# Kernel tuning notes

Measured on AMD Instinct MI355X. Metric: run time of the kernel, lower is better.

The kernel has to match this reference:

```python
import jax, jax.numpy as jnp
import numpy as np

B, N, K, D, H = 4, 8192, 16, 128, 4
DK = D // H  # key_dim = num_hiddens // num_heads
NEG_INF = -1e9


def setup_inputs() -> dict:
    key = jax.random.key(0)
    ks = jax.random.split(key, 16)
    s = 1.0 / np.sqrt(D)
    return {
        "vertex_feat": jax.random.normal(ks[0], (B, N, D), dtype=jnp.float32),
        "neighbors_idx": jax.random.randint(ks[1], (B, N, K), 0, N, dtype=jnp.int32),
        "valid_lens": jax.random.randint(ks[2], (B, N), 0, K, dtype=jnp.int32),
        # MultiHeadAttention projections (keras EinsumDense with bias)
        "Wq": (jax.random.normal(ks[3], (D, H, DK)) * s).astype(jnp.float32),
        "bq": jnp.zeros((H, DK), jnp.float32),
        "Wk": (jax.random.normal(ks[4], (D, H, DK)) * s).astype(jnp.float32),
        "bk": jnp.zeros((H, DK), jnp.float32),
        "Wv": (jax.random.normal(ks[5], (D, H, DK)) * s).astype(jnp.float32),
        "bv": jnp.zeros((H, DK), jnp.float32),
        "Wo": (jax.random.normal(ks[6], (H, DK, D)) * s).astype(jnp.float32),
        "bo": jnp.zeros((D,), jnp.float32),
        # MLP: Dense(D, relu) -> Dense(D)
        "W1": (jax.random.normal(ks[7], (D, D)) * s).astype(jnp.float32),
        "b1": jnp.zeros((D,), jnp.float32),
        "W2": (jax.random.normal(ks[8], (D, D)) * s).astype(jnp.float32),
        "b2": jnp.zeros((D,), jnp.float32),
    }


def reference(vertex_feat, neighbors_idx, valid_lens,
              Wq, bq, Wk, bk, Wv, bv, Wo, bo, W1, b1, W2, b2):
    # query: [B, N, 1, D]; gathered neighbors (batch_dims=1): [B, N, K, D]
    q = vertex_feat[:, :, None, :]
    neigh = jax.vmap(lambda vf, idx: vf[idx])(vertex_feat, neighbors_idx)
    value = jnp.concatenate([q, neigh], axis=2)  # [B, N, K+1, D]

    # per-head projections
    qh = jnp.einsum('bnqd,dhk->bnqhk', q, Wq) + bq      # [B,N,1,H,DK]
    kh = jnp.einsum('bnsd,dhk->bnshk', value, Wk) + bk  # [B,N,K+1,H,DK]
    vh = jnp.einsum('bnsd,dhk->bnshk', value, Wv) + bv

    # attention over the neighbor axis (attention_axes=(2,))
    scores = jnp.einsum('bnqhk,bnshk->bnhqs', qh, kh) / np.sqrt(DK)  # [B,N,H,1,K+1]
    # mask: positions < valid_lens + 1 (self + valid neighbors)
    pos = jnp.arange(K + 1)[None, None, :]                # [1,1,K+1]
    mask = pos < (valid_lens + 1)[:, :, None]             # [B,N,K+1] bool
    scores = scores + jnp.where(mask, 0.0, NEG_INF)[:, :, None, None, :]
    attn = jax.nn.softmax(scores, axis=-1)                # [B,N,H,1,K+1]

    ctx = jnp.einsum('bnhqs,bnshk->bnqhk', attn, vh)      # [B,N,1,H,DK]
    out = jnp.einsum('bnqhk,hkd->bnqd', ctx, Wo) + bo     # [B,N,1,D]
    out = out[:, :, 0, :]                                  # squeeze -> [B,N,D]

    # MLP (dropout inactive at inference)
    h = jax.nn.relu(out @ W1 + b1)
    new_vertex_feat = h @ W2 + b2
    return new_vertex_feat
```

## Files before the change

kernel.cpp:

```cpp
#include <hip/hip_runtime.h>
#include <math.h>

#define BB 4
#define NN 8192
#define KNB 16
#define DD 128
#define SS 17
#define M_TOT (BB*NN)
#define WPAD 136

typedef __attribute__((ext_vector_type(8))) short          bf8;
typedef __attribute__((ext_vector_type(4))) float          f4;
typedef __attribute__((ext_vector_type(4))) unsigned short u16x4;

static __device__ __forceinline__ unsigned short f2bf(float f) {
    unsigned u = __builtin_bit_cast(unsigned, f);
    u += 0x7fffu + ((u >> 16) & 1u);
    return (unsigned short)(u >> 16);
}
static __device__ __forceinline__ float bf2f(unsigned short h) {
    return __builtin_bit_cast(float, (unsigned)h << 16);
}
static __device__ __forceinline__ float bf2f_s(short h) {
    return __builtin_bit_cast(float, (unsigned)(unsigned short)h << 16);
}

__global__ __launch_bounds__(256) void cvt_wT(
    const float* __restrict__ Wq, const float* __restrict__ Wk,
    const float* __restrict__ Wv, const float* __restrict__ Wo,
    const float* __restrict__ W1, const float* __restrict__ W2,
    unsigned short* __restrict__ out)
{
    int m = blockIdx.x >> 4;
    const float* src = (m == 0) ? Wq : (m == 1) ? Wk : (m == 2) ? Wv
                     : (m == 3) ? Wo : (m == 4) ? W1 : W2;
    unsigned short* dst = out + m * 16384;
    int o = (blockIdx.x & 15) * 1024 + threadIdx.x * 4;
    int n = o >> 7, k = o & 127;
    u16x4 r;
    #pragma unroll
    for (int i = 0; i < 4; ++i) r[i] = f2bf(src[(size_t)(k + i) * 128 + n]);
    *(u16x4*)(dst + o) = r;
}

__global__ __launch_bounds__(256) void qkv_kernel(
    const float* __restrict__ X, const unsigned short* __restrict__ WtT,
    const float* __restrict__ bq, const float* __restrict__ bk,
    const float* __restrict__ bv,
    unsigned short* __restrict__ qh, unsigned short* __restrict__ kh,
    unsigned short* __restrict__ vh)
{
    __shared__ unsigned short Xs[64 * WPAD];
    __shared__ unsigned short Wb[128 * WPAD];

    const int tid  = threadIdx.x;
    const int row0 = blockIdx.x * 64;

    {
        const float4* Xg = (const float4*)(X + (size_t)row0 * DD);
        #pragma unroll
        for (int i = 0; i < 8; ++i) {
            int idx = tid + i * 256;
            int r = idx >> 5, c4 = idx & 31;
            float4 v = Xg[idx];
            u16x4 u;
            u[0] = f2bf(v.x); u[1] = f2bf(v.y); u[2] = f2bf(v.z); u[3] = f2bf(v.w);
            *(u16x4*)(Xs + r * WPAD + c4 * 4) = u;
        }
    }
    #pragma unroll
    for (int i = 0; i < 8; ++i) {
        int c = tid + i * 256;
        int n = c >> 4, k8 = c & 15;
        *(bf8*)(Wb + n * WPAD + k8 * 8) = ((const bf8*)WtT)[c];
    }

    const int lane = tid & 63, wv = tid >> 6;
    const int ln = lane & 15, quad = lane >> 4;
    __syncthreads();

    bf8 afr[4];
    #pragma unroll
    for (int s = 0; s < 4; ++s)
        afr[s] = *(const bf8*)(Xs + (wv * 16 + ln) * WPAD + s * 32 + quad * 8);

    const float* biases[3] = { bq, bk, bv };
    unsigned short* outs[3] = { qh, kh, vh };

    #pragma unroll 1
    for (int g = 0; g < 3; ++g) {
        if (g > 0) {
            __syncthreads();
            const bf8* Wn = (const bf8*)(WtT + g * 16384);
            #pragma unroll
            for (int i = 0; i < 8; ++i) {
                int c = tid + i * 256;
                int n = c >> 4, k8 = c & 15;
                *(bf8*)(Wb + n * WPAD + k8 * 8) = Wn[c];
            }
            __syncthreads();
        }

        f4 acc[8] = {};
        #pragma unroll
        for (int t = 0; t < 8; ++t) {
            bf8 bfr[4];
            #pragma unroll
            for (int s = 0; s < 4; ++s)
                bfr[s] = *(const bf8*)(Wb + (t * 16 + ln) * WPAD + s * 32 + quad * 8);
            #pragma unroll
            for (int s = 0; s < 4; ++s)
                acc[t] = __builtin_amdgcn_mfma_f32_16x16x32_bf16(afr[s], bfr[s], acc[t], 0, 0, 0);
        }

        const float* bias = biases[g];
        unsigned short* Y = outs[g];
        #pragma unroll
        for (int t = 0; t < 8; ++t) {
            int col = t * 16 + ln;
            float bc = bias[col];
            #pragma unroll
            for (int r = 0; r < 4; ++r) {
                int row = row0 + wv * 16 + quad * 4 + r;
                Y[(size_t)row * DD + col] = f2bf(acc[t][r] + bc);
            }
        }
    }
}

__global__ __launch_bounds__(256) void attn_kernel(
    const unsigned short* __restrict__ Qh, const unsigned short* __restrict__ Kh,
    const unsigned short* __restrict__ Vh, const int* __restrict__ nbr,
    const int* __restrict__ vlen, unsigned short* __restrict__ Ctx)
{
    const int tid  = threadIdx.x;
    const int vloc = tid >> 4;
    const int ln   = tid & 15;
    const int blk  = blockIdx.x;
    const int b    = (blk & 7) >> 1;
    const int j    = ((blk >> 3) << 1) | (blk & 1);
    const int v    = b * NN + j * 16 + vloc;

    bf8 q8 = *(const bf8*)(Qh + (size_t)v * DD + ln * 8);
    float qf[8];
    #pragma unroll
    for (int i = 0; i < 8; ++i) qf[i] = bf2f_s(q8[i]);

    int rows[SS];
    rows[0] = v;
    {
        const int4* np = (const int4*)(nbr + (size_t)v * KNB);
        #pragma unroll
        for (int i = 0; i < 4; ++i) {
            int4 n4 = np[i];
            rows[1 + i * 4 + 0] = b * NN + n4.x;
            rows[1 + i * 4 + 1] = b * NN + n4.y;
            rows[1 + i * 4 + 2] = b * NN + n4.z;
            rows[1 + i * 4 + 3] = b * NN + n4.w;
        }
    }

    float sc[SS];
    #pragma unroll
    for (int s = 0; s < SS; ++s) {
        bf8 k8 = *(const bf8*)(Kh + (size_t)rows[s] * DD + ln * 8);
        float p = 0.f;
        #pragma unroll
        for (int i = 0; i < 8; ++i) p = fmaf(qf[i], bf2f_s(k8[i]), p);
        p += __shfl_xor(p, 1, 4);
        p += __shfl_xor(p, 2, 4);
        sc[s] = p * 0.17677669529663687f;
    }

    const int len = vlen[v];
    float m = sc[0];
    #pragma unroll
    for (int s = 1; s < SS; ++s) m = (s <= len) ? fmaxf(m, sc[s]) : m;
    float sum = 0.f;
    #pragma unroll
    for (int s = 0; s < SS; ++s) {
        float e = (s <= len) ? __expf(sc[s] - m) : 0.f;
        sc[s] = e;
        sum += e;
    }
    const float inv = 1.f / sum;

    float acc[8] = {};
    #pragma unroll
    for (int s = 0; s < SS; ++s) {
        bf8 v8 = *(const bf8*)(Vh + (size_t)rows[s] * DD + ln * 8);
        float w = sc[s] * inv;
        #pragma unroll
        for (int i = 0; i < 8; ++i) acc[i] = fmaf(w, bf2f_s(v8[i]), acc[i]);
    }
    bf8 r;
    #pragma unroll
    for (int i = 0; i < 8; ++i) r[i] = (short)f2bf(acc[i]);
    *(bf8*)(Ctx + (size_t)v * DD + ln * 8) = r;
}

__global__ __launch_bounds__(256) void ffn_kernel(
    const unsigned short* __restrict__ Ctxg, const unsigned short* __restrict__ WtT3,
    const float* __restrict__ bo, const float* __restrict__ b1,
    const float* __restrict__ b2, float* __restrict__ Out)
{
    __shared__ unsigned short Ct[64 * WPAD];
    __shared__ unsigned short Wb[128 * WPAD];

    const int tid  = threadIdx.x;
    const int row0 = blockIdx.x * 64;

    {
        const bf8* Cg = (const bf8*)(Ctxg + (size_t)row0 * DD);
        #pragma unroll
        for (int i = 0; i < 4; ++i) {
            int idx = tid + i * 256;
            int r = idx >> 4, c8 = idx & 15;
            *(bf8*)(Ct + r * WPAD + c8 * 8) = Cg[idx];
        }
    }
    #pragma unroll
    for (int i = 0; i < 8; ++i) {
        int c = tid + i * 256;
        int n = c >> 4, k8 = c & 15;
        *(bf8*)(Wb + n * WPAD + k8 * 8) = ((const bf8*)WtT3)[c];
    }

    const int lane = tid & 63, wv = tid >> 6;
    const int ln = lane & 15, quad = lane >> 4;
    const float* biases[3] = { bo, b1, b2 };
    __syncthreads();

    #pragma unroll 1
    for (int g = 0; g < 3; ++g) {
        bf8 afr[4];
        #pragma unroll
        for (int s = 0; s < 4; ++s)
            afr[s] = *(const bf8*)(Ct + (wv * 16 + ln) * WPAD + s * 32 + quad * 8);

        f4 acc[8] = {};
        #pragma unroll
        for (int t = 0; t < 8; ++t) {
            bf8 bfr[4];
            #pragma unroll
            for (int s = 0; s < 4; ++s)
                bfr[s] = *(const bf8*)(Wb + (t * 16 + ln) * WPAD + s * 32 + quad * 8);
            #pragma unroll
            for (int s = 0; s < 4; ++s)
                acc[t] = __builtin_amdgcn_mfma_f32_16x16x32_bf16(afr[s], bfr[s], acc[t], 0, 0, 0);
        }

        __syncthreads();

        const float* bias = biases[g];
        if (g == 2) {
            #pragma unroll
            for (int t = 0; t < 8; ++t) {
                int col = t * 16 + ln;
                float bc = bias[col];
                #pragma unroll
                for (int r = 0; r < 4; ++r) {
                    int row = row0 + wv * 16 + quad * 4 + r;
                    Out[(size_t)row * DD + col] = acc[t][r] + bc;
                }
            }
        } else {
            const bf8* Wn = (const bf8*)(WtT3 + (g + 1) * 16384);
            #pragma unroll
            for (int i = 0; i < 8; ++i) {
                int c = tid + i * 256;
                int n = c >> 4, k8 = c & 15;
                *(bf8*)(Wb + n * WPAD + k8 * 8) = Wn[c];
            }
            #pragma unroll
            for (int t = 0; t < 8; ++t) {
                int col = t * 16 + ln;
                float bc = bias[col];
                #pragma unroll
                for (int r = 0; r < 4; ++r) {
                    int rloc = wv * 16 + quad * 4 + r;
                    float vv = acc[t][r] + bc;
                    if (g == 1) vv = fmaxf(vv, 0.f);
                    Ct[rloc * WPAD + col] = f2bf(vv);
                }
            }
            __syncthreads();
        }
    }
}

extern "C" void kernel_launch(void* const* d_in, const int* in_sizes, int n_in,
                              void* d_out, int out_size, void* d_ws, size_t ws_size,
                              hipStream_t stream)
{
    const float* vf   = (const float*)d_in[0];
    const int*   nbr  = (const int*)  d_in[1];
    const int*   vlen = (const int*)  d_in[2];
    const float* Wq   = (const float*)d_in[3];
    const float* bq   = (const float*)d_in[4];
    const float* Wk   = (const float*)d_in[5];
    const float* bk   = (const float*)d_in[6];
    const float* Wv   = (const float*)d_in[7];
    const float* bv   = (const float*)d_in[8];
    const float* Wo   = (const float*)d_in[9];
    const float* bo   = (const float*)d_in[10];
    const float* W1   = (const float*)d_in[11];
    const float* b1   = (const float*)d_in[12];
    const float* W2   = (const float*)d_in[13];
    const float* b2   = (const float*)d_in[14];

    float* out = (float*)d_out;

    const size_t SZ = (size_t)M_TOT * DD;
    unsigned short* WtT = (unsigned short*)d_ws;
    unsigned short* qh  = WtT + 6 * 16384;
    unsigned short* kh  = qh + SZ;
    unsigned short* vh  = kh + SZ;
    unsigned short* ctx = vh + SZ;

    cvt_wT<<<96, 256, 0, stream>>>(Wq, Wk, Wv, Wo, W1, W2, WtT);

    qkv_kernel<<<M_TOT / 64, 256, 0, stream>>>(vf, WtT, bq, bk, bv, qh, kh, vh);

    attn_kernel<<<M_TOT / 16, 256, 0, stream>>>(qh, kh, vh, nbr, vlen, ctx);

    ffn_kernel<<<M_TOT / 64, 256, 0, stream>>>(ctx, WtT + 3 * 16384, bo, b1, b2, out);
}
```

Baseline: 134.8 us.

## Interleave K and V rows and split neighbor set across two thread halves

The QKV kernel now writes K and V interleaved into one 256-wide row, so each gathered neighbor's K and V share a contiguous 512-byte region. The attention kernel splits the 17 key/value slots between two 16-lane halves per vertex (9 each, with the self row duplicated and masked out in one half). The halves combine max, sum and context through cross-lane shuffles, and the grid doubles to 8 vertices per block. This aims to raise memory-level parallelism and cut per-thread serial gather latency, at the cost of redundant Q loads, extra shuffles and half the threads idle on the store.

```diff
diff --git a/kernel.cpp b/kernel.cpp
--- a/kernel.cpp
+++ b/kernel.cpp
@@ -18,9 +18,6 @@
     u += 0x7fffu + ((u >> 16) & 1u);
     return (unsigned short)(u >> 16);
 }
-static __device__ __forceinline__ float bf2f(unsigned short h) {
-    return __builtin_bit_cast(float, (unsigned)h << 16);
-}
 static __device__ __forceinline__ float bf2f_s(short h) {
     return __builtin_bit_cast(float, (unsigned)(unsigned short)h << 16);
 }
@@ -47,8 +44,7 @@
     const float* __restrict__ X, const unsigned short* __restrict__ WtT,
     const float* __restrict__ bq, const float* __restrict__ bk,
     const float* __restrict__ bv,
-    unsigned short* __restrict__ qh, unsigned short* __restrict__ kh,
-    unsigned short* __restrict__ vh)
+    unsigned short* __restrict__ qh, unsigned short* __restrict__ kv)
 {
     __shared__ unsigned short Xs[64 * WPAD];
     __shared__ unsigned short Wb[128 * WPAD];
@@ -85,7 +81,8 @@
         afr[s] = *(const bf8*)(Xs + (wv * 16 + ln) * WPAD + s * 32 + quad * 8);
 
     const float* biases[3] = { bq, bk, bv };
-    unsigned short* outs[3] = { qh, kh, vh };
+    unsigned short* outs[3] = { qh, kv, kv + 128 };
+    const int strides[3] = { 128, 256, 256 };
 
     #pragma unroll 1
     for (int g = 0; g < 3; ++g) {
@@ -115,6 +112,7 @@
 
         const float* bias = biases[g];
         unsigned short* Y = outs[g];
+        const int st = strides[g];
         #pragma unroll
         for (int t = 0; t < 8; ++t) {
             int col = t * 16 + ln;
@@ -122,81 +120,96 @@
             #pragma unroll
             for (int r = 0; r < 4; ++r) {
                 int row = row0 + wv * 16 + quad * 4 + r;
-                Y[(size_t)row * DD + col] = f2bf(acc[t][r] + bc);
+                Y[(size_t)row * st + col] = f2bf(acc[t][r] + bc);
             }
         }
     }
 }
 
 __global__ __launch_bounds__(256) void attn_kernel(
-    const unsigned short* __restrict__ Qh, const unsigned short* __restrict__ Kh,
-    const unsigned short* __restrict__ Vh, const int* __restrict__ nbr,
-    const int* __restrict__ vlen, unsigned short* __restrict__ Ctx)
+    const unsigned short* __restrict__ Qh, const unsigned short* __restrict__ KV,
+    const int* __restrict__ nbr, const int* __restrict__ vlen,
+    unsigned short* __restrict__ Ctx)
 {
     const int tid  = threadIdx.x;
-    const int vloc = tid >> 4;
-    const int ln   = tid & 15;
+    const int vloc = tid >> 5;
+    const int sp   = (tid >> 4) & 1;
+    const int ln16 = tid & 15;
     const int blk  = blockIdx.x;
     const int b    = (blk & 7) >> 1;
     const int j    = ((blk >> 3) << 1) | (blk & 1);
-    const int v    = b * NN + j * 16 + vloc;
-
-    bf8 q8 = *(const bf8*)(Qh + (size_t)v * DD + ln * 8);
+    const int v    = b * NN + j * 8 + vloc;
+    const int len  = vlen[v];
+
+    bf8 q8 = *(const bf8*)(Qh + (size_t)v * DD + ln16 * 8);
     float qf[8];
     #pragma unroll
     for (int i = 0; i < 8; ++i) qf[i] = bf2f_s(q8[i]);
 
-    int rows[SS];
-    rows[0] = v;
+    int rows[9];
     {
         const int4* np = (const int4*)(nbr + (size_t)v * KNB);
-        #pragma unroll
-        for (int i = 0; i < 4; ++i) {
-            int4 n4 = np[i];
-            rows[1 + i * 4 + 0] = b * NN + n4.x;
-            rows[1 + i * 4 + 1] = b * NN + n4.y;
-            rows[1 + i * 4 + 2] = b * NN + n4.z;
-            rows[1 + i * 4 + 3] = b * NN + n4.w;
-        }
-    }
-
-    float sc[SS];
-    #pragma unroll
-    for (int s = 0; s < SS; ++s) {
-        bf8 k8 = *(const bf8*)(Kh + (size_t)rows[s] * DD + ln * 8);
+        if (sp == 0) {
+            rows[0] = v;
+            int4 a = np[0], c = np[1];
+            rows[1] = b * NN + a.x; rows[2] = b * NN + a.y;
+            rows[3] = b * NN + a.z; rows[4] = b * NN + a.w;
+            rows[5] = b * NN + c.x; rows[6] = b * NN + c.y;
+            rows[7] = b * NN + c.z; rows[8] = b * NN + c.w;
+        } else {
+            int4 a = np[2], c = np[3];
+            rows[0] = b * NN + a.x; rows[1] = b * NN + a.y;
+            rows[2] = b * NN + a.z; rows[3] = b * NN + a.w;
+            rows[4] = b * NN + c.x; rows[5] = b * NN + c.y;
+            rows[6] = b * NN + c.z; rows[7] = b * NN + c.w;
+            rows[8] = v;
+        }
+    }
+    const int s0 = sp * 9;
+
+    float sc[9];
+    #pragma unroll
+    for (int i = 0; i < 9; ++i) {
+        bf8 k8 = *(const bf8*)(KV + (size_t)rows[i] * 256 + ln16 * 8);
         float p = 0.f;
         #pragma unroll
-        for (int i = 0; i < 8; ++i) p = fmaf(qf[i], bf2f_s(k8[i]), p);
+        for (int d = 0; d < 8; ++d) p = fmaf(qf[d], bf2f_s(k8[d]), p);
         p += __shfl_xor(p, 1, 4);
         p += __shfl_xor(p, 2, 4);
-        sc[s] = p * 0.17677669529663687f;
-    }
-
-    const int len = vlen[v];
+        sc[i] = (s0 + i <= len) ? p * 0.17677669529663687f : -1.0e9f;
+    }
+
     float m = sc[0];
     #pragma unroll
-    for (int s = 1; s < SS; ++s) m = (s <= len) ? fmaxf(m, sc[s]) : m;
+    for (int i = 1; i < 9; ++i) m = fmaxf(m, sc[i]);
+    m = fmaxf(m, __shfl_xor(m, 16));
     float sum = 0.f;
     #pragma unroll
-    for (int s = 0; s < SS; ++s) {
-        float e = (s <= len) ? __expf(sc[s] - m) : 0.f;
-        sc[s] = e;
+    for (int i = 0; i < 9; ++i) {
+        float e = __expf(sc[i] - m);
+        sc[i] = e;
         sum += e;
     }
+    sum += __shfl_xor(sum, 16);
     const float inv = 1.f / sum;
 
     float acc[8] = {};
     #pragma unroll
-    for (int s = 0; s < SS; ++s) {
-        bf8 v8 = *(const bf8*)(Vh + (size_t)rows[s] * DD + ln * 8);
-        float w = sc[s] * inv;
-        #pragma unroll
-        for (int i = 0; i < 8; ++i) acc[i] = fmaf(w, bf2f_s(v8[i]), acc[i]);
-    }
-    bf8 r;
-    #pragma unroll
-    for (int i = 0; i < 8; ++i) r[i] = (short)f2bf(acc[i]);
-    *(bf8*)(Ctx + (size_t)v * DD + ln * 8) = r;
+    for (int i = 0; i < 9; ++i) {
+        bf8 v8 = *(const bf8*)(KV + (size_t)rows[i] * 256 + 128 + ln16 * 8);
+        float w = sc[i] * inv;
+        #pragma unroll
+        for (int d = 0; d < 8; ++d) acc[d] = fmaf(w, bf2f_s(v8[d]), acc[d]);
+    }
+    #pragma unroll
+    for (int d = 0; d < 8; ++d) acc[d] += __shfl_xor(acc[d], 16);
+
+    if (sp == 0) {
+        bf8 r;
+        #pragma unroll
+        for (int d = 0; d < 8; ++d) r[d] = (short)f2bf(acc[d]);
+        *(bf8*)(Ctx + (size_t)v * DD + ln16 * 8) = r;
+    }
 }
 
 __global__ __launch_bounds__(256) void ffn_kernel(
@@ -314,15 +327,14 @@
     const size_t SZ = (size_t)M_TOT * DD;
     unsigned short* WtT = (unsigned short*)d_ws;
     unsigned short* qh  = WtT + 6 * 16384;
-    unsigned short* kh  = qh + SZ;
-    unsigned short* vh  = kh + SZ;
-    unsigned short* ctx = vh + SZ;
+    unsigned short* kv  = qh + SZ;
+    unsigned short* ctx = kv + 2 * SZ;
 
     cvt_wT<<<96, 256, 0, stream>>>(Wq, Wk, Wv, Wo, W1, W2, WtT);
 
-    qkv_kernel<<<M_TOT / 64, 256, 0, stream>>>(vf, WtT, bq, bk, bv, qh, kh, vh);
-
-    attn_kernel<<<M_TOT / 16, 256, 0, stream>>>(qh, kh, vh, nbr, vlen, ctx);
+    qkv_kernel<<<M_TOT / 64, 256, 0, stream>>>(vf, WtT, bq, bk, bv, qh, kv);
+
+    attn_kernel<<<M_TOT / 8, 256, 0, stream>>>(qh, kv, nbr, vlen, ctx);
 
     ffn_kernel<<<M_TOT / 64, 256, 0, stream>>>(ctx, WtT + 3 * 16384, bo, b1, b2, out);
 }
```

Measured after the change: 136.0 us. About the same (+0.9%).
